# Performance work log

Measured on AMD Instinct MI355X. Metric: run time of the kernel, lower is better.

## Reference

```python
import jax, jax.numpy as jnp
import numpy as np

S = 2          # scale_int = ceil(scale)
K = 3          # kernel size
OUTC = 3       # num_out_ch
NUM_FEAT = 64


def conv3x3(x, w, b):
    y = jax.lax.conv_general_dilated(x, w, (1, 1), ((1, 1), (1, 1)),
                                     dimension_numbers=('NCHW', 'OIHW', 'NCHW'))
    return y + b[None, :, None, None]


def unfold3x3(x):
    # torch F.unfold(x, 3, padding=1): (N, C*9, H*W), order c*9 + ki*3 + kj
    N, C, H, W = x.shape
    xp = jnp.pad(x, ((0, 0), (0, 0), (1, 1), (1, 1)))
    patches = jnp.stack([xp[:, :, i:i + H, j:j + W]
                         for i in range(3) for j in range(3)], axis=2)  # (N,C,9,H,W)
    return patches.reshape(N, C * 9, H * W)


def setup_inputs() -> dict:
    key = jax.random.key(0)
    ks = jax.random.split(key, 12)
    b, t, c, h, w = 2, 4, 16, 64, 64
    H, W = S * h, S * w
    nf4 = 64 // 4  # 16
    d_w = K * K * NUM_FEAT * OUTC  # 1728
    return {
        'x0': jax.random.normal(ks[0], (b, NUM_FEAT, h, w), jnp.float32),
        'feature': jax.random.normal(ks[1], (b, t, c, h, w), jnp.float32),
        'pos_mat': jax.random.uniform(ks[2], (H, W, 3), jnp.float32),
        'mask': jnp.ones((b, OUTC, H, W), dtype=bool),
        'conv1_w': jax.random.normal(ks[3], (nf4, 64, 3, 3), jnp.float32) * 0.05,
        'conv1_b': jnp.zeros((nf4,), jnp.float32),
        'conv2_w': jax.random.normal(ks[4], (nf4, nf4, 3, 3), jnp.float32) * 0.05,
        'conv2_b': jnp.zeros((nf4,), jnp.float32),
        'f2w1_w': jax.random.normal(ks[5], (256, nf4 + 1), jnp.float32) * 0.05,
        'f2w1_b': jnp.zeros((256,), jnp.float32),
        'f2w2_w': jax.random.normal(ks[6], (d_w, 256), jnp.float32) * 0.05,
        'f2w2_b': jnp.zeros((d_w,), jnp.float32),
    }


def reference(x0, feature, pos_mat, mask, conv1_w, conv1_b, conv2_w, conv2_b,
              f2w1_w, f2w1_b, f2w2_w, f2w2_b):
    b, t, c, h, w = feature.shape
    H, W = S * h, S * w
    # with_gradBack=False -> feature.detach()
    feat = jax.lax.stop_gradient(feature).reshape(b, t * c, h, w)
    # repeat_x(..., upsample=True): nearest-neighbour upsample by S
    feat_up = jnp.repeat(jnp.repeat(feat, S, axis=2), S, axis=3)  # (b,64,H,W)
    f = jax.nn.relu(conv3x3(feat_up, conv1_w, conv1_b))
    f = conv3x3(f, conv2_w, conv2_b)                              # (b,16,H,W)
    pos0 = jnp.transpose(pos_mat, (2, 0, 1))[0:1]                 # (1,H,W)
    fm = jnp.concatenate([f, jnp.broadcast_to(pos0[None], (b, 1, H, W))], axis=1)
    fm = fm.reshape(b, -1, H * W).transpose(0, 2, 1)              # (b,HW,17)
    hdn = jax.nn.relu(fm @ f2w1_w.T + f2w1_b)
    weights = hdn @ f2w2_w.T + f2w2_b                             # (b,HW,1728)
    weights = weights.reshape(b, h, S, w, S, K * K * NUM_FEAT, OUTC)
    weights = jnp.transpose(weights, (0, 2, 4, 1, 3, 5, 6))
    weights = weights.reshape(b, S * S, h * w, K * K * NUM_FEAT, OUTC)
    # repeat_x(x0) tiles x0 S^2 times -> all S^2 col copies identical; compute once
    cols = unfold3x3(x0).transpose(0, 2, 1)                       # (b,hw,576)
    out = jnp.einsum('bpk,bspko->bspo', cols, weights)            # (b,S^2,hw,3)
    out = jnp.transpose(out, (0, 1, 3, 2)).reshape(b, S, S, OUTC, h, w)
    out = jnp.transpose(out, (0, 3, 4, 1, 5, 2)).reshape(b, OUTC, H, W)
    # integer scale -> mask all True -> masked_select + view is identity
    return out, weights
```

## Files before the change

kernel.cpp:

```cpp
#include <hip/hip_runtime.h>

#define THREADS 256

#define Bsz 2
#define HWp 16384
#define Ntot (Bsz*HWp)
#define HID 256
#define Mm 1728
#define FMC 17
#define W_OFF 98304

#define F1_OFF  16384
#define F1_SZ   (Bsz*16*HWp)
#define FM_OFF  (F1_OFF + F1_SZ)

typedef __attribute__((ext_vector_type(8))) short bf16x8;
typedef __attribute__((ext_vector_type(4))) float f32x4;

static __device__ __forceinline__ short f2bf(float x) {
    unsigned u = __builtin_bit_cast(unsigned, x);
    unsigned r = (u + 0x7fff + ((u >> 16) & 1)) >> 16;
    return (short)r;
}

__global__ __launch_bounds__(THREADS) void k1_conv1(const float* __restrict__ feat,
                                                    const float* __restrict__ w1,
                                                    const float* __restrict__ b1,
                                                    float* __restrict__ f1) {
    __shared__ float sW[4 * 64 * 4];
    int tid = threadIdx.x;
    int t = blockIdx.x * THREADS + tid;
    int c = t & 63, r = (t >> 6) & 63, oc = (t >> 12) & 15, bb = t >> 16;

    #pragma unroll
    for (int q = 0; q < 4; ++q) {
        int e = tid * 4 + q;
        int v = e & 1, u = (e >> 1) & 1, ic = (e >> 2) & 63, pp = (e >> 8) & 3;
        int pi = pp >> 1, pj = pp & 1;
        float s = 0.f;
        for (int ki = 0; ki < 3; ++ki) {
            bool okki = pi ? (u ? (ki == 2) : (ki <= 1)) : (u ? (ki >= 1) : (ki == 0));
            if (!okki) continue;
            for (int kj = 0; kj < 3; ++kj) {
                bool okkj = pj ? (v ? (kj == 2) : (kj <= 1)) : (v ? (kj >= 1) : (kj == 0));
                if (okkj) s += w1[((oc * 64 + ic) * 3 + ki) * 3 + kj];
            }
        }
        sW[(pp * 64 + ic) * 4 + u * 2 + v] = s;
    }
    __syncthreads();

    float bias = b1[oc];
    float acc00 = bias, acc01 = bias, acc10 = bias, acc11 = bias;

    float my0 = (r > 0) ? 1.f : 0.f, my2 = (r < 63) ? 1.f : 0.f;
    float mx0 = (c > 0) ? 1.f : 0.f, mx2 = (c < 63) ? 1.f : 0.f;
    float m00 = my0 * mx0, m01 = my0, m02 = my0 * mx2;
    float m10 = mx0,       m12 = mx2;
    float m20 = my2 * mx0, m21 = my2, m22 = my2 * mx2;
    int ro0 = (r > 0) ? -64 : 0, ro2 = (r < 63) ? 64 : 0;
    int co0 = (c > 0) ? -1 : 0,  co2 = (c < 63) ? 1 : 0;

    const float* fb = feat + bb * 64 * 4096 + r * 64 + c;
    for (int ic = 0; ic < 64; ++ic) {
        const float* p1 = fb + ic * 4096;
        const float* p0 = p1 + ro0;
        const float* p2 = p1 + ro2;
        float v00 = p0[co0] * m00, v01 = p0[0] * m01, v02 = p0[co2] * m02;
        float v10 = p1[co0] * m10, v11 = p1[0],       v12 = p1[co2] * m12;
        float v20 = p2[co0] * m20, v21 = p2[0] * m21, v22 = p2[co2] * m22;

        f32x4 w0 = *(const f32x4*)(sW + (0 * 64 + ic) * 4);
        f32x4 w1v = *(const f32x4*)(sW + (1 * 64 + ic) * 4);
        f32x4 w2v = *(const f32x4*)(sW + (2 * 64 + ic) * 4);
        f32x4 w3 = *(const f32x4*)(sW + (3 * 64 + ic) * 4);

        acc00 = fmaf(w0[0], v00, acc00); acc00 = fmaf(w0[1], v01, acc00);
        acc00 = fmaf(w0[2], v10, acc00); acc00 = fmaf(w0[3], v11, acc00);
        acc01 = fmaf(w1v[0], v01, acc01); acc01 = fmaf(w1v[1], v02, acc01);
        acc01 = fmaf(w1v[2], v11, acc01); acc01 = fmaf(w1v[3], v12, acc01);
        acc10 = fmaf(w2v[0], v10, acc10); acc10 = fmaf(w2v[1], v11, acc10);
        acc10 = fmaf(w2v[2], v20, acc10); acc10 = fmaf(w2v[3], v21, acc10);
        acc11 = fmaf(w3[0], v11, acc11); acc11 = fmaf(w3[1], v12, acc11);
        acc11 = fmaf(w3[2], v21, acc11); acc11 = fmaf(w3[3], v22, acc11);
    }

    float* fo = f1 + (bb * 16 + oc) * HWp + (2 * r) * 128 + 2 * c;
    float2 r0 = make_float2(fmaxf(acc00, 0.f), fmaxf(acc01, 0.f));
    float2 r1 = make_float2(fmaxf(acc10, 0.f), fmaxf(acc11, 0.f));
    *reinterpret_cast<float2*>(fo) = r0;
    *reinterpret_cast<float2*>(fo + 128) = r1;
}

__global__ __launch_bounds__(THREADS) void k2_conv2_fm(const float* __restrict__ f1,
                                                       const float* __restrict__ w2,
                                                       const float* __restrict__ b2,
                                                       const float* __restrict__ pos,
                                                       float* __restrict__ fm) {
    int t = blockIdx.x * THREADS + threadIdx.x;
    if (t >= Bsz * FMC * HWp) return;
    int J = t & 127, I = (t >> 7) & 127;
    int bc = t >> 14;
    int ch = bc % FMC, bb = bc / FMC;
    int n = bb * HWp + I * 128 + J;
    float val;
    if (ch == 16) {
        val = pos[(I * 128 + J) * 3];
    } else {
        float acc = b2[ch];
        for (int ic = 0; ic < 16; ++ic) {
            const float* fb = f1 + (bb * 16 + ic) * HWp;
            const float* wb = w2 + (ch * 16 + ic) * 9;
            for (int ki = 0; ki < 3; ++ki) {
                int y = I + ki - 1;
                if ((unsigned)y >= 128u) continue;
                const float* row = fb + y * 128;
                for (int kj = 0; kj < 3; ++kj) {
                    int x = J + kj - 1;
                    if ((unsigned)x >= 128u) continue;
                    acc = fmaf(row[x], wb[ki * 3 + kj], acc);
                }
            }
        }
        val = acc;
    }
    fm[n * FMC + ch] = val;
}

__global__ __launch_bounds__(THREADS) void k3_cvtB(const float* __restrict__ w2g,
                                                   short* __restrict__ wB2) {
    int t = blockIdx.x * THREADS + threadIdx.x;
    int i = t & 7, l = (t >> 3) & 63, ct = (t >> 9) & 3, s = (t >> 11) & 7, mc = t >> 14;
    int col = mc * 64 + ct * 16 + (l & 15);
    int k = s * 32 + (l >> 4) * 8 + i;
    wB2[t] = f2bf(w2g[col * HID + k]);
}

__global__ __launch_bounds__(THREADS, 2) void k4_gemm(const float* __restrict__ fm,
                                                      const float* __restrict__ w1g,
                                                      const float* __restrict__ b1g,
                                                      const short* __restrict__ wB2,
                                                      const float* __restrict__ b2g,
                                                      const float* __restrict__ x0g,
                                                      float* __restrict__ dout) {
    __shared__ short    sA[16384];
    __shared__ float    sFM[64 * 20];
    __shared__ int      sOB[64];
    __shared__ float    sX[6528];
    __shared__ unsigned sLUT[1792];
    __shared__ float    sOut[4 * 64 * 3];

    int tid = threadIdx.x;
    int n0 = blockIdx.x * 64;
    int bb = n0 >> 14, tt = n0 & 16383, I = tt >> 7, J0 = tt & 127;
    int i0 = I >> 1, jmin = J0 >> 1;

    for (int idx = tid; idx < 64 * FMC; idx += THREADS) {
        int r = idx / FMC, i2 = idx - r * FMC;
        sFM[r * 20 + i2] = fm[n0 * FMC + idx];
    }
    if (tid < 64) {
        int J = J0 + tid;
        int s = ((I & 1) << 1) | (J & 1);
        int p = ((I >> 1) << 6) | (J >> 1);
        sOB[tid] = W_OFF + ((bb * 4 + s) * 4096 + p) * Mm;
    }
    for (int m = tid; m < Mm; m += THREADS) {
        int k = m / 3;
        int ch = k / 9, rem = k - ch * 9;
        int ki = rem / 3, kj = rem - ki * 3;
        sLUT[m] = (unsigned)((ch * 3 + ki) * 34 + kj);
    }
    {
        const float* x0b = x0g + bb * 64 * 4096;
        for (int e = tid; e < 6528; e += THREADS) {
            int ch = e / 102, r2 = e - ch * 102;
            int ki = r2 / 34, jc = r2 - ki * 34;
            int y = i0 + ki - 1, x = jmin + jc - 1;
            float v = 0.f;
            if ((unsigned)y < 64u && (unsigned)x < 64u) v = x0b[(ch * 64 + y) * 64 + x];
            sX[e] = v;
        }
    }
    __syncthreads();

    {
        float wreg[FMC];
        #pragma unroll
        for (int i = 0; i < FMC; ++i) wreg[i] = w1g[tid * FMC + i];
        float bj = b1g[tid];
        int g = (tid >> 3) & 7;
        int base = (tid >> 3) * 512 + (tid & 7);
        for (int rr = 0; rr < 64; ++rr) {
            int r = (rr + g) & 63;
            const float* fr = sFM + r * 20;
            f32x4 x0 = *(const f32x4*)fr;
            f32x4 x1 = *(const f32x4*)(fr + 4);
            f32x4 x2 = *(const f32x4*)(fr + 8);
            f32x4 x3 = *(const f32x4*)(fr + 12);
            float s = fmaf(fr[16], wreg[16], bj);
            s = fmaf(x0[0], wreg[0], s);  s = fmaf(x0[1], wreg[1], s);
            s = fmaf(x0[2], wreg[2], s);  s = fmaf(x0[3], wreg[3], s);
            s = fmaf(x1[0], wreg[4], s);  s = fmaf(x1[1], wreg[5], s);
            s = fmaf(x1[2], wreg[6], s);  s = fmaf(x1[3], wreg[7], s);
            s = fmaf(x2[0], wreg[8], s);  s = fmaf(x2[1], wreg[9], s);
            s = fmaf(x2[2], wreg[10], s); s = fmaf(x2[3], wreg[11], s);
            s = fmaf(x3[0], wreg[12], s); s = fmaf(x3[1], wreg[13], s);
            s = fmaf(x3[2], wreg[14], s); s = fmaf(x3[3], wreg[15], s);
            sA[base + r * 8] = f2bf(fmaxf(s, 0.f));
        }
    }
    __syncthreads();

    int wid = tid >> 6, l = tid & 63;
    int lm = l & 15, lg = l >> 4;
    int lg3 = lg % 3;

    int pixbase[4], jl[4];
    #pragma unroll
    for (int rt = 0; rt < 4; ++rt) {
        pixbase[rt] = sOB[rt * 16 + lm];
        jl[rt] = rt * 8 + (lm >> 1);
    }

    const short* aptr = sA + lg * 512 + lm * 8;

    float racc[4][3];
    #pragma unroll
    for (int rt = 0; rt < 4; ++rt) {
        racc[rt][0] = 0.f; racc[rt][1] = 0.f; racc[rt][2] = 0.f;
    }

    for (int mc = wid; mc < 27; mc += 4) {
        int m0 = mc * 64;
        f32x4 acc[4][4];
        #pragma unroll
        for (int ct = 0; ct < 4; ++ct) {
            f32x4 bias4 = *(const f32x4*)(b2g + m0 + ct * 16 + lg * 4);
            #pragma unroll
            for (int rt = 0; rt < 4; ++rt)
                acc[rt][ct] = bias4;
        }
        const short* bbase = wB2 + (size_t)mc * 16384 + l * 8;
        #pragma unroll 2
        for (int s = 0; s < 8; ++s) {
            bf16x8 af[4], bfr[4];
            #pragma unroll
            for (int rt = 0; rt < 4; ++rt)
                af[rt] = *(const bf16x8*)(aptr + s * 2048 + rt * 128);
            #pragma unroll
            for (int ct = 0; ct < 4; ++ct)
                bfr[ct] = *(const bf16x8*)(bbase + (s * 4 + ct) * 512);
            #pragma unroll
            for (int rt = 0; rt < 4; ++rt)
                #pragma unroll
                for (int ct = 0; ct < 4; ++ct)
                    acc[rt][ct] = __builtin_amdgcn_mfma_f32_16x16x32_bf16(
                        bfr[ct], af[rt], acc[rt][ct], 0, 0, 0);
        }
        #pragma unroll
        for (int rt = 0; rt < 4; ++rt)
            #pragma unroll
            for (int ct = 0; ct < 4; ++ct)
                *(f32x4*)(dout + pixbase[rt] + m0 + ct * 16 + lg * 4) = acc[rt][ct];
        unsigned lutv[4];
#define ACCUM(QB)                                                              \
        _Pragma("unroll")                                                      \
        for (int ct = 0; ct < 4; ++ct) {                                       \
            *(uint4*)lutv = *(const uint4*)(sLUT + m0 + ct * 16 + lg * 4);     \
            _Pragma("unroll")                                                  \
            for (int r = 0; r < 4; ++r) {                                      \
                _Pragma("unroll")                                              \
                for (int rt = 0; rt < 4; ++rt) {                               \
                    float v = sX[lutv[r] + jl[rt]];                            \
                    racc[rt][((QB) + ct + r) % 3] =                            \
                        fmaf(acc[rt][ct][r], v, racc[rt][((QB) + ct + r) % 3]);\
                }                                                              \
            }                                                                  \
        }
        switch (mc % 3) {
            case 0: ACCUM(0); break;
            case 1: ACCUM(1); break;
            default: ACCUM(2); break;
        }
#undef ACCUM
    }

    #pragma unroll
    for (int rt = 0; rt < 4; ++rt) {
        float q0 = racc[rt][0], q1 = racc[rt][1], q2 = racc[rt][2];
        float a0 = (lg3 == 0) ? q0 : ((lg3 == 1) ? q2 : q1);
        float a1 = (lg3 == 0) ? q1 : ((lg3 == 1) ? q0 : q2);
        float a2 = (lg3 == 0) ? q2 : ((lg3 == 1) ? q1 : q0);
        a0 += __shfl_xor(a0, 16, 64); a0 += __shfl_xor(a0, 32, 64);
        a1 += __shfl_xor(a1, 16, 64); a1 += __shfl_xor(a1, 32, 64);
        a2 += __shfl_xor(a2, 16, 64); a2 += __shfl_xor(a2, 32, 64);
        if (l < 16) {
            float* so = sOut + (wid * 64 + rt * 16 + lm) * 3;
            so[0] = a0; so[1] = a1; so[2] = a2;
        }
    }
    __syncthreads();
    if (tid < 192) {
        float s = sOut[tid] + sOut[192 + tid] + sOut[384 + tid] + sOut[576 + tid];
        int pix = tid / 3, o = tid - 3 * pix;
        dout[bb * 3 * HWp + o * HWp + I * 128 + J0 + pix] = s;
    }
}

extern "C" void kernel_launch(void* const* d_in, const int* in_sizes, int n_in,
                              void* d_out, int out_size, void* d_ws, size_t ws_size,
                              hipStream_t stream) {
    const float* x0      = (const float*)d_in[0];
    const float* feature = (const float*)d_in[1];
    const float* pos     = (const float*)d_in[2];
    const float* w1      = (const float*)d_in[4];
    const float* b1      = (const float*)d_in[5];
    const float* w2      = (const float*)d_in[6];
    const float* b2      = (const float*)d_in[7];
    const float* f2w1_w  = (const float*)d_in[8];
    const float* f2w1_b  = (const float*)d_in[9];
    const float* f2w2_w  = (const float*)d_in[10];
    const float* f2w2_b  = (const float*)d_in[11];

    float* out = (float*)d_out;
    float* ws  = (float*)d_ws;
    float* f1  = ws + F1_OFF;
    float* fm  = ws + FM_OFF;
    short* wB2 = (short*)(ws + F1_OFF);

    k1_conv1<<<(Bsz * 16 * 64 * 64) / THREADS, THREADS, 0, stream>>>(feature, w1, b1, f1);
    k2_conv2_fm<<<(Bsz * FMC * HWp) / THREADS, THREADS, 0, stream>>>(f1, w2, b2, pos, fm);
    k3_cvtB<<<(Mm * HID) / THREADS, THREADS, 0, stream>>>(f2w2_w, wB2);
    k4_gemm<<<Ntot / 64, THREADS, 0, stream>>>(fm, f2w1_w, f2w1_b, wB2, f2w2_b, x0, out);
}
```

Measured before the change: 130.2 us.

## Fuse weight conversion into conv1 launch and register-block both convolutions

Moves the bf16 weight conversion into extra blocks of the conv1 kernel, so one launch disappears and the conversion runs alongside conv1. Conv1 now computes two low-res rows per thread (r and r+32), and conv2 computes 8 output channels per thread with branch-free masked halo loads. This cuts per-output recomputation of input loads and the divergent boundary branches. The workspace is re-laid out so wB2 no longer aliases f1, which also removes an ordering dependency. Costs are more registers per thread and fewer threads in the conv kernels.

```diff
diff --git a/kernel.cpp b/kernel.cpp
--- a/kernel.cpp
+++ b/kernel.cpp
@@ -10,9 +10,10 @@
 #define FMC 17
 #define W_OFF 98304
 
-#define F1_OFF  16384
+#define F1_OFF  0
 #define F1_SZ   (Bsz*16*HWp)
-#define FM_OFF  (F1_OFF + F1_SZ)
+#define FM_OFF  F1_SZ
+#define WB2_OFF (FM_OFF + Ntot*FMC)
 
 typedef __attribute__((ext_vector_type(8))) short bf16x8;
 typedef __attribute__((ext_vector_type(4))) float f32x4;
@@ -23,14 +24,27 @@
     return (short)r;
 }
 
-__global__ __launch_bounds__(THREADS) void k1_conv1(const float* __restrict__ feat,
-                                                    const float* __restrict__ w1,
-                                                    const float* __restrict__ b1,
-                                                    float* __restrict__ f1) {
+__global__ __launch_bounds__(THREADS) void k13_conv1_cvt(const float* __restrict__ feat,
+                                                         const float* __restrict__ w1,
+                                                         const float* __restrict__ b1,
+                                                         float* __restrict__ f1,
+                                                         const float* __restrict__ w2g,
+                                                         short* __restrict__ wB2) {
+    int tid = threadIdx.x;
+    if (blockIdx.x >= 256) {
+        int t = (blockIdx.x - 256) * THREADS + tid;
+        int i = t & 7, l = (t >> 3) & 63, ct = (t >> 9) & 3, s = (t >> 11) & 7, mc = t >> 14;
+        int col = mc * 64 + ct * 16 + (l & 15);
+        int k = s * 32 + (l >> 4) * 8 + i;
+        wB2[t] = f2bf(w2g[col * HID + k]);
+        return;
+    }
     __shared__ float sW[4 * 64 * 4];
-    int tid = threadIdx.x;
-    int t = blockIdx.x * THREADS + tid;
-    int c = t & 63, r = (t >> 6) & 63, oc = (t >> 12) & 15, bb = t >> 16;
+    int b = blockIdx.x;
+    int rb = b & 7, oc = (b >> 3) & 15, bb = b >> 7;
+    int c = tid & 63, sr = tid >> 6;
+    int r0 = rb * 4 + sr;
+    int r1 = r0 + 32;
 
     #pragma unroll
     for (int q = 0; q < 4; ++q) {
@@ -51,45 +65,63 @@
     __syncthreads();
 
     float bias = b1[oc];
-    float acc00 = bias, acc01 = bias, acc10 = bias, acc11 = bias;
-
-    float my0 = (r > 0) ? 1.f : 0.f, my2 = (r < 63) ? 1.f : 0.f;
-    float mx0 = (c > 0) ? 1.f : 0.f, mx2 = (c < 63) ? 1.f : 0.f;
-    float m00 = my0 * mx0, m01 = my0, m02 = my0 * mx2;
-    float m10 = mx0,       m12 = mx2;
-    float m20 = my2 * mx0, m21 = my2, m22 = my2 * mx2;
-    int ro0 = (r > 0) ? -64 : 0, ro2 = (r < 63) ? 64 : 0;
-    int co0 = (c > 0) ? -1 : 0,  co2 = (c < 63) ? 1 : 0;
-
-    const float* fb = feat + bb * 64 * 4096 + r * 64 + c;
+    float aA00 = bias, aA01 = bias, aA10 = bias, aA11 = bias;
+    float aB00 = bias, aB01 = bias, aB10 = bias, aB11 = bias;
+
+    float mA = (r0 > 0) ? 1.f : 0.f;
+    float mB = (r1 < 63) ? 1.f : 0.f;
+    float mc0 = (c > 0) ? 1.f : 0.f, mc2 = (c < 63) ? 1.f : 0.f;
+    int roA0 = (r0 > 0) ? -64 : 0;
+    int roB2 = (r1 < 63) ? 64 : 0;
+    int co0 = (c > 0) ? -1 : 0, co2 = (c < 63) ? 1 : 0;
+
+    const float* fbA = feat + bb * 64 * 4096 + r0 * 64 + c;
+    const float* fbB = feat + bb * 64 * 4096 + r1 * 64 + c;
     for (int ic = 0; ic < 64; ++ic) {
-        const float* p1 = fb + ic * 4096;
-        const float* p0 = p1 + ro0;
-        const float* p2 = p1 + ro2;
-        float v00 = p0[co0] * m00, v01 = p0[0] * m01, v02 = p0[co2] * m02;
-        float v10 = p1[co0] * m10, v11 = p1[0],       v12 = p1[co2] * m12;
-        float v20 = p2[co0] * m20, v21 = p2[0] * m21, v22 = p2[co2] * m22;
+        const float* pA1 = fbA + ic * 4096;
+        const float* pA0 = pA1 + roA0;
+        const float* pA2 = pA1 + 64;
+        const float* pB1 = fbB + ic * 4096;
+        const float* pB0 = pB1 - 64;
+        const float* pB2 = pB1 + roB2;
+
+        float vA00 = pA0[co0] * (mA * mc0), vA01 = pA0[0] * mA, vA02 = pA0[co2] * (mA * mc2);
+        float vA10 = pA1[co0] * mc0,        vA11 = pA1[0],      vA12 = pA1[co2] * mc2;
+        float vA20 = pA2[co0] * mc0,        vA21 = pA2[0],      vA22 = pA2[co2] * mc2;
+        float vB00 = pB0[co0] * mc0,        vB01 = pB0[0],      vB02 = pB0[co2] * mc2;
+        float vB10 = pB1[co0] * mc0,        vB11 = pB1[0],      vB12 = pB1[co2] * mc2;
+        float vB20 = pB2[co0] * (mB * mc0), vB21 = pB2[0] * mB, vB22 = pB2[co2] * (mB * mc2);
 
         f32x4 w0 = *(const f32x4*)(sW + (0 * 64 + ic) * 4);
         f32x4 w1v = *(const f32x4*)(sW + (1 * 64 + ic) * 4);
         f32x4 w2v = *(const f32x4*)(sW + (2 * 64 + ic) * 4);
         f32x4 w3 = *(const f32x4*)(sW + (3 * 64 + ic) * 4);
 
-        acc00 = fmaf(w0[0], v00, acc00); acc00 = fmaf(w0[1], v01, acc00);
-        acc00 = fmaf(w0[2], v10, acc00); acc00 = fmaf(w0[3], v11, acc00);
-        acc01 = fmaf(w1v[0], v01, acc01); acc01 = fmaf(w1v[1], v02, acc01);
-        acc01 = fmaf(w1v[2], v11, acc01); acc01 = fmaf(w1v[3], v12, acc01);
-        acc10 = fmaf(w2v[0], v10, acc10); acc10 = fmaf(w2v[1], v11, acc10);
-        acc10 = fmaf(w2v[2], v20, acc10); acc10 = fmaf(w2v[3], v21, acc10);
-        acc11 = fmaf(w3[0], v11, acc11); acc11 = fmaf(w3[1], v12, acc11);
-        acc11 = fmaf(w3[2], v21, acc11); acc11 = fmaf(w3[3], v22, acc11);
-    }
-
-    float* fo = f1 + (bb * 16 + oc) * HWp + (2 * r) * 128 + 2 * c;
-    float2 r0 = make_float2(fmaxf(acc00, 0.f), fmaxf(acc01, 0.f));
-    float2 r1 = make_float2(fmaxf(acc10, 0.f), fmaxf(acc11, 0.f));
-    *reinterpret_cast<float2*>(fo) = r0;
-    *reinterpret_cast<float2*>(fo + 128) = r1;
+        aA00 = fmaf(w0[0], vA00, aA00); aA00 = fmaf(w0[1], vA01, aA00);
+        aA00 = fmaf(w0[2], vA10, aA00); aA00 = fmaf(w0[3], vA11, aA00);
+        aA01 = fmaf(w1v[0], vA01, aA01); aA01 = fmaf(w1v[1], vA02, aA01);
+        aA01 = fmaf(w1v[2], vA11, aA01); aA01 = fmaf(w1v[3], vA12, aA01);
+        aA10 = fmaf(w2v[0], vA10, aA10); aA10 = fmaf(w2v[1], vA11, aA10);
+        aA10 = fmaf(w2v[2], vA20, aA10); aA10 = fmaf(w2v[3], vA21, aA10);
+        aA11 = fmaf(w3[0], vA11, aA11); aA11 = fmaf(w3[1], vA12, aA11);
+        aA11 = fmaf(w3[2], vA21, aA11); aA11 = fmaf(w3[3], vA22, aA11);
+
+        aB00 = fmaf(w0[0], vB00, aB00); aB00 = fmaf(w0[1], vB01, aB00);
+        aB00 = fmaf(w0[2], vB10, aB00); aB00 = fmaf(w0[3], vB11, aB00);
+        aB01 = fmaf(w1v[0], vB01, aB01); aB01 = fmaf(w1v[1], vB02, aB01);
+        aB01 = fmaf(w1v[2], vB11, aB01); aB01 = fmaf(w1v[3], vB12, aB01);
+        aB10 = fmaf(w2v[0], vB10, aB10); aB10 = fmaf(w2v[1], vB11, aB10);
+        aB10 = fmaf(w2v[2], vB20, aB10); aB10 = fmaf(w2v[3], vB21, aB10);
+        aB11 = fmaf(w3[0], vB11, aB11); aB11 = fmaf(w3[1], vB12, aB11);
+        aB11 = fmaf(w3[2], vB21, aB11); aB11 = fmaf(w3[3], vB22, aB11);
+    }
+
+    float* foA = f1 + (bb * 16 + oc) * HWp + (2 * r0) * 128 + 2 * c;
+    *reinterpret_cast<float2*>(foA)       = make_float2(fmaxf(aA00, 0.f), fmaxf(aA01, 0.f));
+    *reinterpret_cast<float2*>(foA + 128) = make_float2(fmaxf(aA10, 0.f), fmaxf(aA11, 0.f));
+    float* foB = f1 + (bb * 16 + oc) * HWp + (2 * r1) * 128 + 2 * c;
+    *reinterpret_cast<float2*>(foB)       = make_float2(fmaxf(aB00, 0.f), fmaxf(aB01, 0.f));
+    *reinterpret_cast<float2*>(foB + 128) = make_float2(fmaxf(aB10, 0.f), fmaxf(aB11, 0.f));
 }
 
 __global__ __launch_bounds__(THREADS) void k2_conv2_fm(const float* __restrict__ f1,
@@ -97,43 +129,43 @@
                                                        const float* __restrict__ b2,
                                                        const float* __restrict__ pos,
                                                        float* __restrict__ fm) {
-    int t = blockIdx.x * THREADS + threadIdx.x;
-    if (t >= Bsz * FMC * HWp) return;
-    int J = t & 127, I = (t >> 7) & 127;
-    int bc = t >> 14;
-    int ch = bc % FMC, bb = bc / FMC;
+    int tid = threadIdx.x;
+    int t = blockIdx.x * THREADS + tid;
+    int J = t & 127, I = (t >> 7) & 127, h = (t >> 14) & 1, bb = t >> 15;
+
+    float acc[8];
+    #pragma unroll
+    for (int o = 0; o < 8; ++o) acc[o] = b2[h * 8 + o];
+
+    int ro0 = (I > 0) ? -128 : 0, ro2 = (I < 127) ? 128 : 0;
+    int co0 = (J > 0) ? -1 : 0, co2 = (J < 127) ? 1 : 0;
+    float mr0 = (I > 0) ? 1.f : 0.f, mr2 = (I < 127) ? 1.f : 0.f;
+    float mcl = (J > 0) ? 1.f : 0.f, mcr = (J < 127) ? 1.f : 0.f;
+
+    const float* fb = f1 + bb * 16 * HWp + I * 128 + J;
+    #pragma unroll 4
+    for (int ic = 0; ic < 16; ++ic) {
+        const float* p1 = fb + ic * HWp;
+        const float* p0 = p1 + ro0;
+        const float* p2 = p1 + ro2;
+        float v0 = p0[co0] * (mr0 * mcl), v1 = p0[0] * mr0, v2 = p0[co2] * (mr0 * mcr);
+        float v3 = p1[co0] * mcl,         v4 = p1[0],       v5 = p1[co2] * mcr;
+        float v6 = p2[co0] * (mr2 * mcl), v7 = p2[0] * mr2, v8 = p2[co2] * (mr2 * mcr);
+        const float* wp = w2 + (h * 8 * 16 + ic) * 9;
+        #pragma unroll
+        for (int o = 0; o < 8; ++o) {
+            const float* w = wp + o * 144;
+            acc[o] = fmaf(v0, w[0], acc[o]); acc[o] = fmaf(v1, w[1], acc[o]);
+            acc[o] = fmaf(v2, w[2], acc[o]); acc[o] = fmaf(v3, w[3], acc[o]);
+            acc[o] = fmaf(v4, w[4], acc[o]); acc[o] = fmaf(v5, w[5], acc[o]);
+            acc[o] = fmaf(v6, w[6], acc[o]); acc[o] = fmaf(v7, w[7], acc[o]);
+            acc[o] = fmaf(v8, w[8], acc[o]);
+        }
+    }
     int n = bb * HWp + I * 128 + J;
-    float val;
-    if (ch == 16) {
-        val = pos[(I * 128 + J) * 3];
-    } else {
-        float acc = b2[ch];
-        for (int ic = 0; ic < 16; ++ic) {
-            const float* fb = f1 + (bb * 16 + ic) * HWp;
-            const float* wb = w2 + (ch * 16 + ic) * 9;
-            for (int ki = 0; ki < 3; ++ki) {
-                int y = I + ki - 1;
-                if ((unsigned)y >= 128u) continue;
-                const float* row = fb + y * 128;
-                for (int kj = 0; kj < 3; ++kj) {
-                    int x = J + kj - 1;
-                    if ((unsigned)x >= 128u) continue;
-                    acc = fmaf(row[x], wb[ki * 3 + kj], acc);
-                }
-            }
-        }
-        val = acc;
-    }
-    fm[n * FMC + ch] = val;
-}
-
-__global__ __launch_bounds__(THREADS) void k3_cvtB(const float* __restrict__ w2g,
-                                                   short* __restrict__ wB2) {
-    int t = blockIdx.x * THREADS + threadIdx.x;
-    int i = t & 7, l = (t >> 3) & 63, ct = (t >> 9) & 3, s = (t >> 11) & 7, mc = t >> 14;
-    int col = mc * 64 + ct * 16 + (l & 15);
-    int k = s * 32 + (l >> 4) * 8 + i;
-    wB2[t] = f2bf(w2g[col * HID + k]);
+    #pragma unroll
+    for (int o = 0; o < 8; ++o) fm[n * FMC + h * 8 + o] = acc[o];
+    if (h == 0) fm[n * FMC + 16] = pos[(I * 128 + J) * 3];
 }
 
 __global__ __launch_bounds__(THREADS, 2) void k4_gemm(const float* __restrict__ fm,
@@ -327,10 +359,9 @@
     float* ws  = (float*)d_ws;
     float* f1  = ws + F1_OFF;
     float* fm  = ws + FM_OFF;
-    short* wB2 = (short*)(ws + F1_OFF);
-
-    k1_conv1<<<(Bsz * 16 * 64 * 64) / THREADS, THREADS, 0, stream>>>(feature, w1, b1, f1);
-    k2_conv2_fm<<<(Bsz * FMC * HWp) / THREADS, THREADS, 0, stream>>>(f1, w2, b2, pos, fm);
-    k3_cvtB<<<(Mm * HID) / THREADS, THREADS, 0, stream>>>(f2w2_w, wB2);
+    short* wB2 = (short*)(ws + WB2_OFF);
+
+    k13_conv1_cvt<<<256 + 1728, THREADS, 0, stream>>>(feature, w1, b1, f1, f2w2_w, wB2);
+    k2_conv2_fm<<<(Bsz * 2 * HWp) / THREADS, THREADS, 0, stream>>>(f1, w2, b2, pos, fm);
     k4_gemm<<<Ntot / 64, THREADS, 0, stream>>>(fm, f2w1_w, f2w1_b, wB2, f2w2_b, x0, out);
 }
```

New measurement: 123.8 us. -5.0%, faster.
